# Performance work log

Hardware: AMD Instinct MI355X
Metric: run time of the kernel (lower is better)

Reference implementation:

```python
import jax, jax.numpy as jnp
import numpy as np

N = 64        # SSM state size
L = 262144    # l_max / sequence length


def setup_inputs() -> dict:
    key = jax.random.key(0)
    ks = jax.random.split(key, 8)
    u = jax.random.normal(ks[0], (L,), dtype=jnp.float32)
    # HiPPO-DPLR style eigenvalue init
    Lambda_re = -0.5 * jnp.ones((N,), jnp.float32)
    Lambda_im = jnp.pi * jnp.arange(N, dtype=jnp.float32)
    P_re = jax.random.normal(ks[1], (N,), jnp.float32)
    P_im = jax.random.normal(ks[2], (N,), jnp.float32)
    B_re = jax.random.normal(ks[3], (N,), jnp.float32)
    B_im = jax.random.normal(ks[4], (N,), jnp.float32)
    C_ri = (0.5 ** 0.5) * jax.random.normal(ks[5], (N, 2), jnp.float32)  # C = C_ri[:,0] + i*C_ri[:,1]
    D = jnp.ones((1,), jnp.float32)
    log_step = jax.random.uniform(ks[6], (1,), jnp.float32,
                                  minval=float(np.log(0.001)), maxval=float(np.log(0.1)))
    return {"u": u, "Lambda_re": Lambda_re, "Lambda_im": Lambda_im,
            "P_re": P_re, "P_im": P_im, "B_re": B_re, "B_im": B_im,
            "C_ri": C_ri, "D": D, "log_step": log_step}


def _kernel_DPLR(Lambda, P, Q, B, C, step, l):
    # Evaluate the SSM generating function at the l roots of unity (bilinear discretization)
    Omega = jnp.exp((-2j * jnp.pi) * (jnp.arange(l) / l))          # (L,)
    g = (2.0 / step) * ((1.0 - Omega) / (1.0 + Omega))             # (L,)
    c = 2.0 / (1.0 + Omega)                                        # (L,)
    # Core Cauchy matrix: the single large (L, N) complex intermediate
    recip = 1.0 / (g[:, None] - Lambda[None, :])                   # (L, N)
    # Four Cauchy dot products fused into one thin matmul
    v = jnp.stack([C.conj() * B, C.conj() * P,
                   Q.conj() * B, Q.conj() * P], axis=1)            # (N, 4)
    k = recip @ v                                                  # (L, 4)
    k00, k01, k10, k11 = k[:, 0], k[:, 1], k[:, 2], k[:, 3]
    atRoots = c * (k00 - k01 * (1.0 / (1.0 + k11)) * k10)          # (L,)
    return jnp.fft.ifft(atRoots, l).real                           # (L,) real kernel


def _causal_convolution(u, K):
    l = u.shape[0]
    ud = jnp.fft.rfft(jnp.pad(u, (0, K.shape[0])))
    Kd = jnp.fft.rfft(jnp.pad(K, (0, l)))
    return jnp.fft.irfft(ud * Kd)[:l]


def reference(u, Lambda_re, Lambda_im, P_re, P_im, B_re, B_im, C_ri, D, log_step):
    Lambda = Lambda_re + 1j * Lambda_im
    P = P_re + 1j * P_im
    B = B_re + 1j * B_im
    C = C_ri[:, 0] + 1j * C_ri[:, 1]
    step = jnp.exp(log_step)                                       # (1,)
    K = _kernel_DPLR(Lambda, P, P, B, C, step, u.shape[0])
    return _causal_convolution(u, K) + D * u
```

## Files before the change

### kernel.cpp

```cpp
#include <hip/hip_runtime.h>
#include <math.h>

#define L_LEN  262144
#define NST    64
#define TPB    256
#define TSTR   544
#define PI2F   6.2831853071795864769f
#define PIF    3.1415926535897932385f
#define R2C    0.70710678118654752440f

__device__ inline float2 cmul(float2 a, float2 b) {
    return make_float2(a.x*b.x - a.y*b.y, a.x*b.y + a.y*b.x);
}
__device__ inline float frcp(float x) { return __builtin_amdgcn_rcpf(x); }
__device__ inline float2 cadd(float2 a, float2 b) { return make_float2(a.x+b.x, a.y+b.y); }
__device__ inline float2 csub(float2 a, float2 b) { return make_float2(a.x-b.x, a.y-b.y); }

__device__ inline void twt_init(float2* twt) {
    for (int i = threadIdx.x; i < 576; i += TPB) {
        float ang;
        if (i < 64) ang = PI2F * (float)((i >> 3) * (i & 7)) * (1.0f / 64.0f);
        else { int ii = i - 64;
               ang = PI2F * (float)((ii >> 3) * (ii & 7)) * (1.0f / 512.0f); }
        float sn, cs; __sincosf(ang, &sn, &cs);
        twt[i] = make_float2(cs, sn);
    }
}

template<int M, int NF>
__device__ float2* lds_fft_r8(float2* b0, float2* b1, float sgn, const float2* twt) {
    float2* src = b0; float2* dst = b1;
    for (int Ns = 1; Ns * 8 <= M; Ns <<= 3) {
        __syncthreads();
        const int NB = NF * (M / 8);
        for (int bi = threadIdx.x; bi < NB; bi += TPB) {
            int f = bi / (M / 8);
            int j = bi & (M / 8 - 1);
            int r = j & (Ns - 1);
            const float2* s = src + f * M;
            float2 x[8];
            #pragma unroll
            for (int q = 0; q < 8; ++q) x[q] = s[j + q * (M / 8)];
            if (Ns > 1) {
                const float2* tw = twt + ((Ns == 8) ? 0 : 64) + (r << 3);
                #pragma unroll
                for (int q = 1; q < 8; ++q) {
                    float2 w = tw[q];
                    float wc = w.x, ws = sgn * w.y;
                    x[q] = make_float2(x[q].x*wc - x[q].y*ws,
                                       x[q].x*ws + x[q].y*wc);
                }
            }
            float2 E[4], O[4];
            {
                float2 t0 = cadd(x[0], x[4]), t1 = csub(x[0], x[4]);
                float2 t2 = cadd(x[2], x[6]), t3 = csub(x[2], x[6]);
                E[0] = cadd(t0, t2); E[2] = csub(t0, t2);
                float2 it3 = make_float2(-sgn * t3.y, sgn * t3.x);
                E[1] = cadd(t1, it3); E[3] = csub(t1, it3);
            }
            {
                float2 t0 = cadd(x[1], x[5]), t1 = csub(x[1], x[5]);
                float2 t2 = cadd(x[3], x[7]), t3 = csub(x[3], x[7]);
                O[0] = cadd(t0, t2); O[2] = csub(t0, t2);
                float2 it3 = make_float2(-sgn * t3.y, sgn * t3.x);
                O[1] = cadd(t1, it3); O[3] = csub(t1, it3);
            }
            float2 w1o = make_float2(R2C * (O[1].x - sgn * O[1].y),
                                     R2C * (sgn * O[1].x + O[1].y));
            float2 w2o = make_float2(-sgn * O[2].y, sgn * O[2].x);
            float2 w3o = make_float2(R2C * (-O[3].x - sgn * O[3].y),
                                     R2C * (sgn * O[3].x - O[3].y));
            float2* d = dst + f * M + ((j - r) << 3) + r;
            d[0]      = cadd(E[0], O[0]);
            d[Ns]     = cadd(E[1], w1o);
            d[2 * Ns] = cadd(E[2], w2o);
            d[3 * Ns] = cadd(E[3], w3o);
            d[4 * Ns] = csub(E[0], O[0]);
            d[5 * Ns] = csub(E[1], w1o);
            d[6 * Ns] = csub(E[2], w2o);
            d[7 * Ns] = csub(E[3], w3o);
        }
        float2* tswp = src; src = dst; dst = tswp;
    }
    __syncthreads();
    return src;
}

__global__ __launch_bounds__(TPB, 4) void kI(
    const float* __restrict__ u,
    const float* __restrict__ Lre, const float* __restrict__ Lim,
    const float* __restrict__ Pre, const float* __restrict__ Pim,
    const float* __restrict__ Bre, const float* __restrict__ Bim,
    const float* __restrict__ Cri, const float* __restrict__ lstp,
    float2* __restrict__ Acm, float2* __restrict__ T_K,
    float2* __restrict__ T_U, float2* __restrict__ T_Uo)
{
    __shared__ float2 b0[1024], b1[1024];
    __shared__ float2 twt[576];
    __shared__ float4 cA[NST], cB[NST], cC[NST], cD[NST];
    const int t = threadIdx.x, bx = blockIdx.x;
    const float invL = 1.0f / (float)L_LEN;
    twt_init(twt);
    if (bx < 512) {
        const int c = bx;
        if (t < NST) {
            float lr = Lre[t], li = Lim[t];
            float pr = Pre[t], pi = Pim[t];
            float br = Bre[t], bi = Bim[t];
            float cr = Cri[2*t], ci = Cri[2*t+1];
            float dx = -lr;
            float v00x = cr*br + ci*bi, v00y = cr*bi - ci*br;
            float v01x = cr*pr + ci*pi, v01y = cr*pi - ci*pr;
            float v10x = pr*br + pi*bi, v10y = pr*bi - pi*br;
            float v11x = pr*pr + pi*pi;
            cA[t] = make_float4(li, dx*dx, dx*v11x, -v11x);
            cB[t] = make_float4(dx*v00x, v00y, dx*v00y, -v00x);
            cC[t] = make_float4(dx*v01x, v01y, dx*v01y, -v01x);
            cD[t] = make_float4(dx*v10x, v10y, dx*v10y, -v10x);
        }
        __syncthreads();
        float G2 = 2.0f / expf(lstp[0]);
        float tn[2], gi[2], acc[2][8];
        #pragma unroll
        for (int p = 0; p < 2; ++p) {
            int e = t + (p << 8);
            int m = c + (e << 9);
            float h = PIF * ((float)m * invL);
            float sn, cs; __sincosf(h, &sn, &cs);
            float tv = sn * frcp(cs);
            tv = fminf(fmaxf(tv, -1e7f), 1e7f);
            tn[p] = tv; gi[p] = G2 * tv;
            #pragma unroll
            for (int q = 0; q < 8; ++q) acc[p][q] = 0.f;
        }
        #pragma unroll 2
        for (int n = 0; n < NST; ++n) {
            float4 a = cA[n], b = cB[n], cc = cC[n], d = cD[n];
            #pragma unroll
            for (int p = 0; p < 2; ++p) {
                float dy   = gi[p] - a.x;
                float iv   = frcp(fmaf(dy, dy, a.y));
                float ivdy = iv * dy;
                acc[p][6] = fmaf(iv, a.z, acc[p][6]);
                acc[p][7] = fmaf(ivdy, a.w, acc[p][7]);
                acc[p][0] = fmaf(iv, b.x,  fmaf(ivdy, b.y,  acc[p][0]));
                acc[p][1] = fmaf(iv, b.z,  fmaf(ivdy, b.w,  acc[p][1]));
                acc[p][2] = fmaf(iv, cc.x, fmaf(ivdy, cc.y, acc[p][2]));
                acc[p][3] = fmaf(iv, cc.z, fmaf(ivdy, cc.w, acc[p][3]));
                acc[p][4] = fmaf(iv, d.x,  fmaf(ivdy, d.y,  acc[p][4]));
                acc[p][5] = fmaf(iv, d.z,  fmaf(ivdy, d.w,  acc[p][5]));
            }
        }
        #pragma unroll
        for (int p = 0; p < 2; ++p) {
            int e = t + (p << 8);
            float ax = 1.f + acc[p][6], ay = acc[p][7];
            float im = frcp(ax*ax + ay*ay);
            float tx = acc[p][2]*acc[p][4] - acc[p][3]*acc[p][5];
            float ty = acc[p][2]*acc[p][5] + acc[p][3]*acc[p][4];
            float wx = acc[p][0] - (tx*ax + ty*ay) * im;
            float wy = acc[p][1] - (ty*ax - tx*ay) * im;
            float2 A = make_float2(wx - tn[p]*wy, wy + tn[p]*wx);
            Acm[(c << 9) + e] = A;
            b0[e] = A;
        }
        float2* rA = lds_fft_r8<512, 1>(b0, b1, +1.f, twt);
        for (int k = t; k < 512; k += TPB) {
            float ang = PI2F * ((float)(c * k) * invL);
            float sn, cs; __sincosf(ang, &sn, &cs);
            T_K[k * TSTR + c] = cmul(make_float2(cs, sn), rA[k]);
        }
    } else {
        const int c = bx - 512;
        float uv0 = u[c + (t << 9)];
        float uv1 = u[c + ((t + 256) << 9)];
        {
            int n0 = c + (t << 9), n1 = c + ((t + 256) << 9);
            float sn, cs;
            __sincosf(PIF * ((float)n0 * invL), &sn, &cs);
            b0[t]        = make_float2(uv0, 0.f);
            b0[512 + t]  = make_float2(uv0 * cs, -uv0 * sn);
            __sincosf(PIF * ((float)n1 * invL), &sn, &cs);
            b0[t + 256]       = make_float2(uv1, 0.f);
            b0[512 + t + 256] = make_float2(uv1 * cs, -uv1 * sn);
        }
        float2* rU = lds_fft_r8<512, 2>(b0, b1, -1.f, twt);
        for (int i = t; i < 1024; i += TPB) {
            int v = i >> 9, k = i & 511;
            float ang = -PI2F * ((float)(c * k) * invL);
            float sn, cs; __sincosf(ang, &sn, &cs);
            float2 val = cmul(make_float2(cs, sn), rU[(v << 9) + k]);
            if (v == 0) T_U [k * TSTR + c] = val;
            else        T_Uo[k * TSTR + c] = val;
        }
    }
}

__global__ __launch_bounds__(TPB, 4) void kII(
    const float2* __restrict__ T_K, const float2* __restrict__ T_U,
    const float2* __restrict__ T_Uo,
    float2* __restrict__ T_Ko, float2* __restrict__ Ue, float2* __restrict__ Uo)
{
    __shared__ float2 b0[1024], b1[1024];
    __shared__ float2 twt[576];
    const int t = threadIdx.x, bx = blockIdx.x;
    const float invL = 1.0f / (float)L_LEN;
    twt_init(twt);
    if (bx < 512) {
        const int c = bx;
        for (int i = t; i < 512; i += TPB) b0[i] = T_K[c * TSTR + i];
        float2* rK = lds_fft_r8<512, 1>(b0, b1, +1.f, twt);
        float2* o = (rK == b0) ? b1 : b0;
        for (int i = t; i < 512; i += TPB) {
            int n = c + (i << 9);
            float K = rK[i].x * invL;
            float sn, cs; __sincosf(PIF * ((float)n * invL), &sn, &cs);
            o[i] = make_float2(K * cs, -K * sn);
        }
        float2* r2 = lds_fft_r8<512, 1>(o, rK, -1.f, twt);
        for (int k = t; k < 512; k += TPB) {
            float ang = -PI2F * ((float)(c * k) * invL);
            float sn, cs; __sincosf(ang, &sn, &cs);
            T_Ko[k * TSTR + c] = cmul(make_float2(cs, sn), r2[k]);
        }
    } else {
        const int c = (bx & 511);
        const float2* Tin = (bx < 1024) ? T_U : T_Uo;
        float2* Xo        = (bx < 1024) ? Ue  : Uo;
        for (int i = t; i < 512; i += TPB) b0[i] = Tin[c * TSTR + i];
        float2* r = lds_fft_r8<512, 1>(b0, b1, -1.f, twt);
        for (int k = t; k < 512; k += TPB)
            Xo[(c << 9) + k] = r[k];
    }
}

__global__ __launch_bounds__(TPB, 4) void kIII(
    const float2* __restrict__ T_Ko, const float2* __restrict__ Ue,
    const float2* __restrict__ Uo, const float2* __restrict__ Acm,
    float2* __restrict__ T_Ve, float2* __restrict__ T_Vo)
{
    __shared__ float2 b0[1024], b1[1024];
    __shared__ float2 twt[576];
    const int t = threadIdx.x, bx = blockIdx.x;
    const float invL = 1.0f / (float)L_LEN;
    twt_init(twt);
    if (bx < 512) {
        const int kc = bx;
        for (int i = t; i < 512; i += TPB) b0[i] = T_Ko[kc * TSTR + i];
        float2* rKo = lds_fft_r8<512, 1>(b0, b1, -1.f, twt);
        float2* o3 = (rKo == b0) ? b1 : b0;
        for (int i = t; i < 512; i += TPB)
            o3[i] = cmul(Uo[(kc << 9) + i], rKo[i]);
        float2* rV = lds_fft_r8<512, 1>(o3, rKo, +1.f, twt);
        for (int k = t; k < 512; k += TPB) {
            float ang = PI2F * ((float)(kc * k) * invL);
            float sn, cs; __sincosf(ang, &sn, &cs);
            T_Vo[k * TSTR + kc] = cmul(make_float2(cs, sn), rV[k]);
        }
    } else {
        const int kc = bx - 512;
        for (int i = t; i < 512; i += TPB)
            b0[i] = cmul(Ue[(kc << 9) + i], Acm[(kc << 9) + i]);
        float2* rV = lds_fft_r8<512, 1>(b0, b1, +1.f, twt);
        for (int k = t; k < 512; k += TPB) {
            float ang = PI2F * ((float)(kc * k) * invL);
            float sn, cs; __sincosf(ang, &sn, &cs);
            T_Ve[k * TSTR + kc] = cmul(make_float2(cs, sn), rV[k]);
        }
    }
}

__global__ __launch_bounds__(TPB, 4) void kIV(
    const float2* __restrict__ T_Ve, const float2* __restrict__ T_Vo,
    const float* __restrict__ u, const float* __restrict__ Dp,
    float* __restrict__ out)
{
    __shared__ float2 b0[1024], b1[1024];
    __shared__ float2 twt[576];
    const int t = threadIdx.x, k = blockIdx.x;
    const float invL = 1.0f / (float)L_LEN;
    twt_init(twt);
    for (int i = t; i < 512; i += TPB) {
        b0[i]       = T_Ve[k * TSTR + i];
        b0[i + 512] = T_Vo[k * TSTR + i];
    }
    float2* r = lds_fft_r8<512, 2>(b0, b1, +1.f, twt);
    const float sc = 0.5f * invL;
    const float D = Dp[0];
    for (int o1 = t; o1 < 512; o1 += TPB) {
        int n = k + (o1 << 9);
        float sn, cs; __sincosf(PIF * ((float)n * invL), &sn, &cs);
        float2 yE = r[o1];
        float2 yO = r[o1 + 512];
        out[n] = fmaf(D, u[n], (yE.x + cs * yO.x - sn * yO.y) * sc);
    }
}

extern "C" void kernel_launch(void* const* d_in, const int* in_sizes, int n_in,
                              void* d_out, int out_size, void* d_ws, size_t ws_size,
                              hipStream_t stream) {
    const float* u    = (const float*)d_in[0];
    const float* Lre  = (const float*)d_in[1];
    const float* Lim  = (const float*)d_in[2];
    const float* Pre  = (const float*)d_in[3];
    const float* Pim  = (const float*)d_in[4];
    const float* Bre  = (const float*)d_in[5];
    const float* Bim  = (const float*)d_in[6];
    const float* Cri  = (const float*)d_in[7];
    const float* Dp   = (const float*)d_in[8];
    const float* lstp = (const float*)d_in[9];
    float* out = (float*)d_out;

    char* ws = (char*)d_ws;
    float2* Acm  = (float2*)(ws);
    float2* Ue   = (float2*)(ws + 0x200000);
    float2* Uo   = (float2*)(ws + 0x400000);
    float2* T_K  = (float2*)(ws + 0x600000);
    float2* T_U  = (float2*)(ws + 0x820000);
    float2* T_Uo = (float2*)(ws + 0xA40000);
    float2* T_Ko = (float2*)(ws + 0xC60000);
    float2* T_Ve = (float2*)(ws + 0xE80000);
    float2* T_Vo = (float2*)(ws + 0x10A0000);

    kI  <<<1024, TPB, 0, stream>>>(u, Lre,Lim,Pre,Pim,Bre,Bim,Cri,lstp,
                                   Acm, T_K, T_U, T_Uo);
    kII <<<1536, TPB, 0, stream>>>(T_K, T_U, T_Uo, T_Ko, Ue, Uo);
    kIII<<<1024, TPB, 0, stream>>>(T_Ko, Ue, Uo, Acm, T_Ve, T_Vo);
    kIV <<< 512, TPB, 0, stream>>>(T_Ve, T_Vo, u, Dp, out);
}
```

Measured before the change: 114.8 us.

## Fuse U column FFTs into kIII and batch two K columns per kII block

The second-pass FFTs of the input signal (T_U, T_Uo) move from kII into kIII, where they feed the pointwise products directly. This removes the Ue/Uo workspace buffers and one global write-plus-read round trip per element. kII now handles only the kernel path and processes two columns per block with a batch-2 FFT, launching 256 blocks instead of 1536. The cost is more FFT work per kIII block and fewer, heavier kII blocks, which may underfill the GPU.

```diff
diff --git a/kernel.cpp b/kernel.cpp
--- a/kernel.cpp
+++ b/kernel.cpp
@@ -198,46 +198,38 @@
 }
 
 __global__ __launch_bounds__(TPB, 4) void kII(
-    const float2* __restrict__ T_K, const float2* __restrict__ T_U,
-    const float2* __restrict__ T_Uo,
-    float2* __restrict__ T_Ko, float2* __restrict__ Ue, float2* __restrict__ Uo)
+    const float2* __restrict__ T_K, float2* __restrict__ T_Ko)
 {
     __shared__ float2 b0[1024], b1[1024];
     __shared__ float2 twt[576];
     const int t = threadIdx.x, bx = blockIdx.x;
+    const int c0 = bx << 1;
     const float invL = 1.0f / (float)L_LEN;
     twt_init(twt);
-    if (bx < 512) {
-        const int c = bx;
-        for (int i = t; i < 512; i += TPB) b0[i] = T_K[c * TSTR + i];
-        float2* rK = lds_fft_r8<512, 1>(b0, b1, +1.f, twt);
-        float2* o = (rK == b0) ? b1 : b0;
-        for (int i = t; i < 512; i += TPB) {
-            int n = c + (i << 9);
-            float K = rK[i].x * invL;
-            float sn, cs; __sincosf(PIF * ((float)n * invL), &sn, &cs);
-            o[i] = make_float2(K * cs, -K * sn);
-        }
-        float2* r2 = lds_fft_r8<512, 1>(o, rK, -1.f, twt);
-        for (int k = t; k < 512; k += TPB) {
-            float ang = -PI2F * ((float)(c * k) * invL);
-            float sn, cs; __sincosf(ang, &sn, &cs);
-            T_Ko[k * TSTR + c] = cmul(make_float2(cs, sn), r2[k]);
-        }
-    } else {
-        const int c = (bx & 511);
-        const float2* Tin = (bx < 1024) ? T_U : T_Uo;
-        float2* Xo        = (bx < 1024) ? Ue  : Uo;
-        for (int i = t; i < 512; i += TPB) b0[i] = Tin[c * TSTR + i];
-        float2* r = lds_fft_r8<512, 1>(b0, b1, -1.f, twt);
-        for (int k = t; k < 512; k += TPB)
-            Xo[(c << 9) + k] = r[k];
+    for (int i = t; i < 1024; i += TPB)
+        b0[i] = T_K[(c0 + (i >> 9)) * TSTR + (i & 511)];
+    float2* rK = lds_fft_r8<512, 2>(b0, b1, +1.f, twt);
+    float2* o = (rK == b0) ? b1 : b0;
+    for (int i = t; i < 1024; i += TPB) {
+        int f = i >> 9, e = i & 511;
+        int n = (c0 + f) + (e << 9);
+        float K = rK[i].x * invL;
+        float sn, cs; __sincosf(PIF * ((float)n * invL), &sn, &cs);
+        o[i] = make_float2(K * cs, -K * sn);
+    }
+    float2* r2 = lds_fft_r8<512, 2>(o, rK, -1.f, twt);
+    for (int i = t; i < 1024; i += TPB) {
+        int f = i & 1, k = i >> 1;
+        int c = c0 + f;
+        float ang = -PI2F * ((float)(c * k) * invL);
+        float sn, cs; __sincosf(ang, &sn, &cs);
+        T_Ko[k * TSTR + c] = cmul(make_float2(cs, sn), r2[(f << 9) + k]);
     }
 }
 
 __global__ __launch_bounds__(TPB, 4) void kIII(
-    const float2* __restrict__ T_Ko, const float2* __restrict__ Ue,
-    const float2* __restrict__ Uo, const float2* __restrict__ Acm,
+    const float2* __restrict__ T_Ko, const float2* __restrict__ T_U,
+    const float2* __restrict__ T_Uo, const float2* __restrict__ Acm,
     float2* __restrict__ T_Ve, float2* __restrict__ T_Vo)
 {
     __shared__ float2 b0[1024], b1[1024];
@@ -247,12 +239,15 @@
     twt_init(twt);
     if (bx < 512) {
         const int kc = bx;
-        for (int i = t; i < 512; i += TPB) b0[i] = T_Ko[kc * TSTR + i];
-        float2* rKo = lds_fft_r8<512, 1>(b0, b1, -1.f, twt);
-        float2* o3 = (rKo == b0) ? b1 : b0;
+        for (int i = t; i < 1024; i += TPB) {
+            int f = i >> 9, e = i & 511;
+            b0[i] = f ? T_Uo[kc * TSTR + e] : T_Ko[kc * TSTR + e];
+        }
+        float2* r = lds_fft_r8<512, 2>(b0, b1, -1.f, twt);
+        float2* o3 = (r == b0) ? b1 : b0;
         for (int i = t; i < 512; i += TPB)
-            o3[i] = cmul(Uo[(kc << 9) + i], rKo[i]);
-        float2* rV = lds_fft_r8<512, 1>(o3, rKo, +1.f, twt);
+            o3[i] = cmul(r[512 + i], r[i]);
+        float2* rV = lds_fft_r8<512, 1>(o3, r, +1.f, twt);
         for (int k = t; k < 512; k += TPB) {
             float ang = PI2F * ((float)(kc * k) * invL);
             float sn, cs; __sincosf(ang, &sn, &cs);
@@ -261,8 +256,12 @@
     } else {
         const int kc = bx - 512;
         for (int i = t; i < 512; i += TPB)
-            b0[i] = cmul(Ue[(kc << 9) + i], Acm[(kc << 9) + i]);
-        float2* rV = lds_fft_r8<512, 1>(b0, b1, +1.f, twt);
+            b0[i] = T_U[kc * TSTR + i];
+        float2* r = lds_fft_r8<512, 1>(b0, b1, -1.f, twt);
+        float2* o3 = (r == b0) ? b1 : b0;
+        for (int i = t; i < 512; i += TPB)
+            o3[i] = cmul(r[i], Acm[(kc << 9) + i]);
+        float2* rV = lds_fft_r8<512, 1>(o3, r, +1.f, twt);
         for (int k = t; k < 512; k += TPB) {
             float ang = PI2F * ((float)(kc * k) * invL);
             float sn, cs; __sincosf(ang, &sn, &cs);
@@ -314,18 +313,16 @@
 
     char* ws = (char*)d_ws;
     float2* Acm  = (float2*)(ws);
-    float2* Ue   = (float2*)(ws + 0x200000);
-    float2* Uo   = (float2*)(ws + 0x400000);
-    float2* T_K  = (float2*)(ws + 0x600000);
-    float2* T_U  = (float2*)(ws + 0x820000);
-    float2* T_Uo = (float2*)(ws + 0xA40000);
-    float2* T_Ko = (float2*)(ws + 0xC60000);
-    float2* T_Ve = (float2*)(ws + 0xE80000);
-    float2* T_Vo = (float2*)(ws + 0x10A0000);
+    float2* T_K  = (float2*)(ws + 0x200000);
+    float2* T_U  = (float2*)(ws + 0x420000);
+    float2* T_Uo = (float2*)(ws + 0x640000);
+    float2* T_Ko = (float2*)(ws + 0x860000);
+    float2* T_Ve = (float2*)(ws + 0xA80000);
+    float2* T_Vo = (float2*)(ws + 0xCA0000);
 
     kI  <<<1024, TPB, 0, stream>>>(u, Lre,Lim,Pre,Pim,Bre,Bim,Cri,lstp,
                                    Acm, T_K, T_U, T_Uo);
-    kII <<<1536, TPB, 0, stream>>>(T_K, T_U, T_Uo, T_Ko, Ue, Uo);
-    kIII<<<1024, TPB, 0, stream>>>(T_Ko, Ue, Uo, Acm, T_Ve, T_Vo);
+    kII <<< 256, TPB, 0, stream>>>(T_K, T_Ko);
+    kIII<<<1024, TPB, 0, stream>>>(T_Ko, T_U, T_Uo, Acm, T_Ve, T_Vo);
     kIV <<< 512, TPB, 0, stream>>>(T_Ve, T_Vo, u, Dp, out);
 }
```

Result: no change. 115.1 us (+0.3%).
